# Kernel tuning notes

Hardware: AMD Instinct MI355X
Metric: run time of the kernel (lower is better)

Reference implementation:

```python
import jax, jax.numpy as jnp
import numpy as np


def setup_inputs() -> dict:
    key = jax.random.key(0)
    ks = jax.random.split(key, 8)
    B, C, H, W = 4, 256, 64, 64
    D = C // 8  # query/key dim = 32
    x = jax.random.normal(ks[0], (B, C, H, W), dtype=jnp.float32)
    # 1x1 convs == per-pixel linear maps over channels
    wq = jax.random.normal(ks[1], (D, C), dtype=jnp.float32) * 0.05
    bq = jnp.zeros((D,), dtype=jnp.float32)
    wk = jax.random.normal(ks[2], (D, C), dtype=jnp.float32) * 0.05
    bk = jnp.zeros((D,), dtype=jnp.float32)
    wv = jax.random.normal(ks[3], (C, C), dtype=jnp.float32) * 0.05
    bv = jnp.zeros((C,), dtype=jnp.float32)
    # gamma is initialized to 0 in the original; use a nonzero scalar so the
    # attention path actually contributes to the output / gradients.
    gamma = jnp.array([0.5], dtype=jnp.float32)
    return {"x": x, "wq": wq, "bq": bq, "wk": wk, "bk": bk,
            "wv": wv, "bv": bv, "gamma": gamma}


def reference(x, wq, bq, wk, bk, wv, bv, gamma):
    B, C, H, W = x.shape
    N = H * W
    xf = x.reshape(B, C, N)
    q = jnp.einsum('dc,bcn->bdn', wq, xf) + bq[:, None]   # [B, D, N]
    k = jnp.einsum('dc,bcn->bdn', wk, xf) + bk[:, None]   # [B, D, N]
    v = jnp.einsum('oc,bcn->bon', wv, xf) + bv[:, None]   # [B, C, N]
    # energy[b, i, j] = <q_i, k_j>; softmax over keys j (unscaled, as in source)
    energy = jnp.einsum('bdi,bdj->bij', q, k)             # [B, N, N]
    attn = jax.nn.softmax(energy, axis=-1)
    # out[b, c, j] = sum_i attn[b, i, j] * v[b, c, i]  (transposed aggregation,
    # matching bmm(attention.permute(0,2,1), value.permute(0,2,1)))
    out = jnp.einsum('bij,bci->bcj', attn, v)             # [B, C, N]
    out = out.reshape(B, C, H, W)
    return gamma[0] * out + x
```

## Files before the change

### kernel.cpp

```cpp
#include <hip/hip_runtime.h>

#define NB 4
#define CCH 256
#define NN 4096
#define DD 32

typedef __attribute__((ext_vector_type(8))) short bf16x8;
typedef __attribute__((ext_vector_type(8))) _Float16 f16x8;
typedef __attribute__((ext_vector_type(4))) _Float16 f16x4;
typedef __attribute__((ext_vector_type(2))) __fp16 fp16x2;
typedef __attribute__((ext_vector_type(4))) float f32x4;

#define MFB(a,b,c) __builtin_amdgcn_mfma_f32_16x16x32_bf16(a,b,c,0,0,0)
#define MFH(a,b,c) __builtin_amdgcn_mfma_f32_16x16x32_f16(a,b,c,0,0,0)
#define L2E 1.44269504f

__device__ inline unsigned short f2bf(float f){
    union { float f; unsigned u; } v; v.f = f;
    unsigned r = v.u + 0x7fffu + ((v.u >> 16) & 1u);
    return (unsigned short)(r >> 16);
}
__device__ inline float bfval(unsigned short h){
    union { unsigned u; float f; } v; v.u = ((unsigned)h) << 16; return v.f;
}
__device__ inline float vexp2(float x){
    float r; asm("v_exp_f32 %0, %1" : "=v"(r) : "v"(x)); return r;
}
__device__ inline f16x4 pk4(float p0, float p1, float p2, float p3){
    union { fp16x2 h2[2]; f16x4 v; } u;
    u.h2[0] = __builtin_amdgcn_cvt_pkrtz(p0, p1);
    u.h2[1] = __builtin_amdgcn_cvt_pkrtz(p2, p3);
    return u.v;
}

__global__ __launch_bounds__(256) void proj_qk(
    const float* __restrict__ x,
    const float* __restrict__ wq, const float* __restrict__ bq,
    const float* __restrict__ wk, const float* __restrict__ bk,
    _Float16* __restrict__ q16,
    _Float16* __restrict__ k_hi, _Float16* __restrict__ k_lo)
{
    const int t = threadIdx.x;
    const int w = t >> 6;
    const int l = t & 63;
    const int lr = l & 15, lg = l >> 4;
    const int nb = blockIdx.x;
    const int b  = blockIdx.y;
    const int n0 = nb*64 + w*16;
    const int n  = n0 + lr;

    const float* xb = x + (size_t)b*CCH*NN;

    f32x4 acc[4] = {};

    for (int kc = 0; kc < 8; kc++) {
        const int cbase = kc*32 + lg*8;
        float xv[8];
        #pragma unroll
        for (int e = 0; e < 8; e++)
            xv[e] = xb[(size_t)(cbase + e)*NN + n];
        bf16x8 xh, xl;
        #pragma unroll
        for (int e = 0; e < 8; e++) {
            unsigned short h = f2bf(xv[e]);
            xh[e] = (short)h;
            xl[e] = (short)f2bf(xv[e] - bfval(h));
        }
        #pragma unroll
        for (int f = 0; f < 4; f++) {
            const float* wrow = (f < 2) ? (wq + (size_t)(f*16 + lr)*CCH)
                                        : (wk + (size_t)((f-2)*16 + lr)*CCH);
            float4 a4 = *(const float4*)(wrow + cbase);
            float4 b4 = *(const float4*)(wrow + cbase + 4);
            float wv8[8] = {a4.x,a4.y,a4.z,a4.w,b4.x,b4.y,b4.z,b4.w};
            bf16x8 wh, wl;
            #pragma unroll
            for (int e = 0; e < 8; e++) {
                unsigned short h = f2bf(wv8[e]);
                wh[e] = (short)h;
                wl[e] = (short)f2bf(wv8[e] - bfval(h));
            }
            acc[f] = MFB(xh, wl, acc[f]);
            acc[f] = MFB(xl, wh, acc[f]);
            acc[f] = MFB(xh, wh, acc[f]);
        }
    }

    #pragma unroll
    for (int f = 0; f < 4; f++) {
        const int d = (f & 1)*16 + lr;
        const bool isq = (f < 2);
        float bias = isq ? bq[d] : bk[d];
        #pragma unroll
        for (int r = 0; r < 4; r++) {
            int nn = n0 + lg*4 + r;
            float val = acc[f][r] + bias;
            size_t a = ((size_t)(b*NN + nn))*DD + d;
            if (isq) {
                q16[a] = (_Float16)val;
            } else {
                _Float16 h = (_Float16)val;
                k_hi[a] = h;
                k_lo[a] = (_Float16)(val - (float)h);
            }
        }
    }
}

__global__ __launch_bounds__(512) void proj_v(
    const float* __restrict__ x,
    const float* __restrict__ wv, const float* __restrict__ bv,
    _Float16* __restrict__ v16)
{
    const int t = threadIdx.x;
    const int w = t >> 6;
    const int cg = w >> 2;
    const int ng = w & 3;
    const int l = t & 63;
    const int lr = l & 15, lg = l >> 4;
    const int ob = blockIdx.x;
    const int nb = blockIdx.y;
    const int b  = blockIdx.z;
    const int n0 = nb*64 + ng*16;
    const int n  = n0 + lr;
    const int cbase0 = ob*128 + cg*64;

    const float* xb = x + (size_t)b*CCH*NN;

    f32x4 acc[4] = {};

    for (int kc = 0; kc < 8; kc++) {
        const int kbase = kc*32 + lg*8;
        float xv[8];
        #pragma unroll
        for (int e = 0; e < 8; e++)
            xv[e] = xb[(size_t)(kbase + e)*NN + n];
        bf16x8 xh, xl;
        #pragma unroll
        for (int e = 0; e < 8; e++) {
            unsigned short h = f2bf(xv[e]);
            xh[e] = (short)h;
            xl[e] = (short)f2bf(xv[e] - bfval(h));
        }
        #pragma unroll
        for (int f = 0; f < 4; f++) {
            const float* wrow = wv + (size_t)(cbase0 + f*16 + lr)*CCH;
            float4 a4 = *(const float4*)(wrow + kbase);
            float4 b4 = *(const float4*)(wrow + kbase + 4);
            float wv8[8] = {a4.x,a4.y,a4.z,a4.w,b4.x,b4.y,b4.z,b4.w};
            bf16x8 wh, wl;
            #pragma unroll
            for (int e = 0; e < 8; e++) {
                unsigned short h = f2bf(wv8[e]);
                wh[e] = (short)h;
                wl[e] = (short)f2bf(wv8[e] - bfval(h));
            }
            acc[f] = MFB(wl, xh, acc[f]);
            acc[f] = MFB(wh, xl, acc[f]);
            acc[f] = MFB(wh, xh, acc[f]);
        }
    }

    const size_t bslice = (size_t)b*(NN/8);
    #pragma unroll
    for (int f = 0; f < 4; f++) {
        #pragma unroll
        for (int r = 0; r < 4; r++) {
            int c = cbase0 + f*16 + lg*4 + r;
            float val = acc[f][r] + bv[c];
            v16[(((bslice + (n >> 3))*CCH + c) << 3) + (n & 7)] = (_Float16)val;
        }
    }
}

__global__ __launch_bounds__(512) void stats_kernel(
    const _Float16* __restrict__ q16,
    const _Float16* __restrict__ kh, const _Float16* __restrict__ kl,
    float* __restrict__ Zp)
{
    __shared__ float zW[8][64];
    const int t = threadIdx.x;
    const int w = t >> 6;
    const int l = t & 63;
    const int lr = l & 15, lg = l >> 4;
    const int it = blockIdx.x;
    const int jc = blockIdx.y;
    const int b  = blockIdx.z;
    const int ibase = it*64;
    const f32x4 zero = {0.f,0.f,0.f,0.f};

    f16x8 qf[4];
    #pragma unroll
    for (int f = 0; f < 4; f++) {
        size_t a = ((size_t)(b*NN + ibase + f*16 + lr))*DD + lg*8;
        qf[f] = *(const f16x8*)(q16 + a);
    }
    float Z[4] = {0.f, 0.f, 0.f, 0.f};

    const size_t k0 = ((size_t)(b*NN + jc*2048 + w*16 + lr))*DD + lg*8;
    const _Float16* kp  = kh + k0;
    const _Float16* klp = kl + k0;

    for (int jt = 0; jt < 16; ++jt) {
        f16x8 kh2 = *(const f16x8*)kp;
        f16x8 kl2 = *(const f16x8*)klp;
        #pragma unroll
        for (int f = 0; f < 4; f++) {
            f32x4 e = MFH(kl2, qf[f], zero);
            e = MFH(kh2, qf[f], e);
            Z[f] += vexp2(e[0]*L2E) + vexp2(e[1]*L2E)
                  + vexp2(e[2]*L2E) + vexp2(e[3]*L2E);
        }
        kp  += 128*DD;
        klp += 128*DD;
    }
    #pragma unroll
    for (int f = 0; f < 4; f++) {
        Z[f] += __shfl_xor(Z[f], 16, 64);
        Z[f] += __shfl_xor(Z[f], 32, 64);
        if (lg == 0) zW[w][f*16 + lr] = Z[f];
    }
    __syncthreads();
    if (t < 64) {
        float z = 0.f;
        #pragma unroll
        for (int w2 = 0; w2 < 8; ++w2) z += zW[w2][t];
        Zp[((size_t)jc*NB + b)*NN + ibase + t] = z;
    }
}

__global__ __launch_bounds__(256) void combine_kernel(
    const float* __restrict__ Zp, float* __restrict__ Sx)
{
    const int idx = blockIdx.x*256 + threadIdx.x;
    Sx[idx] = log2f(Zp[idx] + Zp[(size_t)NB*NN + idx]);
}

__global__ __launch_bounds__(256, 2) void attn_kernel(
    const _Float16* __restrict__ q16,
    const _Float16* __restrict__ kh16, const _Float16* __restrict__ kl16,
    const _Float16* __restrict__ v16,
    const float* __restrict__ Sx,
    const float* __restrict__ x, const float* __restrict__ gamma,
    float* __restrict__ out)
{
    __shared__ __align__(16) f32x4 Rb[4096];

    const int t = threadIdx.x;
    const int wv = t >> 6;
    const int l = t & 63;
    const int lr = l & 15, lg = l >> 4;

    const int lin = blockIdx.x;
    const int slice = lin & 7;
    const int b   = slice >> 1;
    const int ct  = slice & 1;
    const int jt  = lin >> 3;
    const int jbase = jt*64, cbase = ct*128;

    f16x8 kfh[4], kfl[4];
    #pragma unroll
    for (int jf = 0; jf < 4; jf++) {
        size_t a = ((size_t)(b*NN + jbase + jf*16 + lr))*DD + lg*8;
        kfh[jf] = *(const f16x8*)(kh16 + a);
        kfl[jf] = *(const f16x8*)(kl16 + a);
    }

    const float* Sb = Sx + (size_t)b*NN;
    const _Float16* vb = v16 + (size_t)b*(NN/8)*CCH*8;

    const int i0 = wv*1024;

    const int sigma = 8*(lr >> 2) + (lr & 3);
    const _Float16* qpA = q16 + ((size_t)(b*NN + i0 + sigma))*DD + lg*8;
    const _Float16* qpB = qpA + 4*DD;
    const float* spA = Sb + i0 + 8*lg;
    const float* spB = spA + 4;
    const _Float16* vp = vb + (((size_t)(i0/8 + lg)*CCH + cbase + lr) << 3);

    f32x4 acc[4][8] = {};

    #pragma clang loop unroll(disable)
    for (int s = 0; s < 32; ++s) {
        f16x8 qA = *(const f16x8*)qpA;  qpA += 32*DD;
        f16x8 qB = *(const f16x8*)qpB;  qpB += 32*DD;
        float4 sA4 = *(const float4*)spA; spA += 32;
        float4 sB4 = *(const float4*)spB; spB += 32;
        f16x8 vv[8];
        #pragma unroll
        for (int cf = 0; cf < 8; cf++)
            vv[cf] = *(const f16x8*)(vp + cf*128);
        vp += 32*CCH;

        #pragma unroll
        for (int jf = 0; jf < 4; jf++) {
            f32x4 eA = {};
            eA = MFH(qA, kfl[jf], eA);
            eA = MFH(qA, kfh[jf], eA);
            f32x4 eB = {};
            eB = MFH(qB, kfl[jf], eB);
            eB = MFH(qB, kfh[jf], eB);
            union { f16x4 h4[2]; f16x8 h8; } pu;
            pu.h4[0] = pk4(vexp2(fmaf(eA[0], L2E, -sA4.x)),
                           vexp2(fmaf(eA[1], L2E, -sA4.y)),
                           vexp2(fmaf(eA[2], L2E, -sA4.z)),
                           vexp2(fmaf(eA[3], L2E, -sA4.w)));
            pu.h4[1] = pk4(vexp2(fmaf(eB[0], L2E, -sB4.x)),
                           vexp2(fmaf(eB[1], L2E, -sB4.y)),
                           vexp2(fmaf(eB[2], L2E, -sB4.z)),
                           vexp2(fmaf(eB[3], L2E, -sB4.w)));
            f16x8 pa = pu.h8;
            __builtin_amdgcn_s_setprio(1);
            #pragma unroll
            for (int cf = 0; cf < 8; cf++)
                acc[jf][cf] = MFH(pa, vv[cf], acc[jf][cf]);
            __builtin_amdgcn_s_setprio(0);
        }
    }

    if (wv == 2) {
        #pragma unroll
        for (int jf = 0; jf < 4; jf++)
            #pragma unroll
            for (int cf = 0; cf < 8; cf++)
                Rb[((jf*8 + cf) << 6) + l] = acc[jf][cf];
    } else if (wv == 3) {
        #pragma unroll
        for (int jf = 0; jf < 4; jf++)
            #pragma unroll
            for (int cf = 0; cf < 8; cf++)
                Rb[2048 + ((jf*8 + cf) << 6) + l] = acc[jf][cf];
    }
    __syncthreads();
    if (wv == 0) {
        #pragma unroll
        for (int jf = 0; jf < 4; jf++)
            #pragma unroll
            for (int cf = 0; cf < 8; cf++)
                acc[jf][cf] += Rb[((jf*8 + cf) << 6) + l];
    } else if (wv == 1) {
        #pragma unroll
        for (int jf = 0; jf < 4; jf++)
            #pragma unroll
            for (int cf = 0; cf < 8; cf++)
                acc[jf][cf] += Rb[2048 + ((jf*8 + cf) << 6) + l];
    }
    __syncthreads();
    if (wv == 0) {
        #pragma unroll
        for (int cf = 0; cf < 8; cf++) {
            Rb[((0*8 + cf) << 6) + l] = acc[2][cf];
            Rb[((1*8 + cf) << 6) + l] = acc[3][cf];
        }
    } else if (wv == 1) {
        #pragma unroll
        for (int cf = 0; cf < 8; cf++) {
            Rb[2048 + ((0*8 + cf) << 6) + l] = acc[0][cf];
            Rb[2048 + ((1*8 + cf) << 6) + l] = acc[1][cf];
        }
    }
    __syncthreads();

    const float gam = gamma[0];
    if (wv == 0) {
        #pragma unroll
        for (int cf = 0; cf < 8; cf++) {
            {
                f32x4 o = Rb[2048 + ((0*8 + cf) << 6) + l];
                f32x4 a = acc[0][cf];
                a[0]+=o[0]; a[1]+=o[1]; a[2]+=o[2]; a[3]+=o[3];
                const int c = cbase + cf*16 + lr;
                const int j = jbase + 0*16 + lg*4;
                size_t off = ((size_t)(b*CCH + c))*NN + j;
                float4 xv = *(const float4*)(x + off);
                float4 ov;
                ov.x = fmaf(gam, a[0], xv.x);
                ov.y = fmaf(gam, a[1], xv.y);
                ov.z = fmaf(gam, a[2], xv.z);
                ov.w = fmaf(gam, a[3], xv.w);
                *(float4*)(out + off) = ov;
            }
            {
                f32x4 o = Rb[2048 + ((1*8 + cf) << 6) + l];
                f32x4 a = acc[1][cf];
                a[0]+=o[0]; a[1]+=o[1]; a[2]+=o[2]; a[3]+=o[3];
                const int c = cbase + cf*16 + lr;
                const int j = jbase + 1*16 + lg*4;
                size_t off = ((size_t)(b*CCH + c))*NN + j;
                float4 xv = *(const float4*)(x + off);
                float4 ov;
                ov.x = fmaf(gam, a[0], xv.x);
                ov.y = fmaf(gam, a[1], xv.y);
                ov.z = fmaf(gam, a[2], xv.z);
                ov.w = fmaf(gam, a[3], xv.w);
                *(float4*)(out + off) = ov;
            }
        }
    } else if (wv == 1) {
        #pragma unroll
        for (int cf = 0; cf < 8; cf++) {
            {
                f32x4 o = Rb[((0*8 + cf) << 6) + l];
                f32x4 a = acc[2][cf];
                a[0]+=o[0]; a[1]+=o[1]; a[2]+=o[2]; a[3]+=o[3];
                const int c = cbase + cf*16 + lr;
                const int j = jbase + 2*16 + lg*4;
                size_t off = ((size_t)(b*CCH + c))*NN + j;
                float4 xv = *(const float4*)(x + off);
                float4 ov;
                ov.x = fmaf(gam, a[0], xv.x);
                ov.y = fmaf(gam, a[1], xv.y);
                ov.z = fmaf(gam, a[2], xv.z);
                ov.w = fmaf(gam, a[3], xv.w);
                *(float4*)(out + off) = ov;
            }
            {
                f32x4 o = Rb[((1*8 + cf) << 6) + l];
                f32x4 a = acc[3][cf];
                a[0]+=o[0]; a[1]+=o[1]; a[2]+=o[2]; a[3]+=o[3];
                const int c = cbase + cf*16 + lr;
                const int j = jbase + 3*16 + lg*4;
                size_t off = ((size_t)(b*CCH + c))*NN + j;
                float4 xv = *(const float4*)(x + off);
                float4 ov;
                ov.x = fmaf(gam, a[0], xv.x);
                ov.y = fmaf(gam, a[1], xv.y);
                ov.z = fmaf(gam, a[2], xv.z);
                ov.w = fmaf(gam, a[3], xv.w);
                *(float4*)(out + off) = ov;
            }
        }
    }
}

extern "C" void kernel_launch(void* const* d_in, const int* in_sizes, int n_in,
                              void* d_out, int out_size, void* d_ws, size_t ws_size,
                              hipStream_t stream)
{
    (void)in_sizes; (void)n_in; (void)out_size; (void)ws_size;
    const float* x     = (const float*)d_in[0];
    const float* wq    = (const float*)d_in[1];
    const float* bq    = (const float*)d_in[2];
    const float* wk    = (const float*)d_in[3];
    const float* bk    = (const float*)d_in[4];
    const float* wv    = (const float*)d_in[5];
    const float* bv    = (const float*)d_in[6];
    const float* gamma = (const float*)d_in[7];
    float* out = (float*)d_out;

    char* ws = (char*)d_ws;
    _Float16* q16  = (_Float16*)(ws + 0x000000);
    _Float16* k_hi = (_Float16*)(ws + 0x100000);
    _Float16* k_lo = (_Float16*)(ws + 0x200000);
    _Float16* v16  = (_Float16*)(ws + 0x400000);
    float*    Zp   = (float*)   (ws + 0xC00000);
    float*    Sx   = (float*)   (ws + 0xC20000);

    proj_qk<<<dim3(64, 4),    256, 0, stream>>>(x, wq, bq, wk, bk,
                                                q16, k_hi, k_lo);
    proj_v <<<dim3(2, 64, 4), 512, 0, stream>>>(x, wv, bv, v16);
    stats_kernel  <<<dim3(64, 2, 4), 512, 0, stream>>>(q16, k_hi, k_lo, Zp);
    combine_kernel<<<dim3(64),       256, 0, stream>>>(Zp, Sx);
    attn_kernel   <<<dim3(512),      256, 0, stream>>>(
        q16, k_hi, k_lo, v16, Sx, x, gamma, out);
}
```

Measured before the change: 118.6 us.

## Pre-split weights to bf16 hi/lo tiles, fuse softmax stats, batch attention MFMAs

Adds a small kernel that converts wq/wk/wv once into MFMA-tiled bf16 hi/lo arrays, so the projection kernels load ready fragments instead of redoing the fp32 split in every block. The stats kernel now covers all keys per block with 32 queries, which removes the partial-sum buffer and the separate combine launch at the cost of a longer serial loop per block. The attention inner loop computes all four P fragments before issuing the 32 PV MFMAs under one priority window, which raises register pressure in exchange for fewer priority toggles and better MFMA back-to-back issue.

```diff
diff --git a/kernel.cpp b/kernel.cpp
--- a/kernel.cpp
+++ b/kernel.cpp
@@ -33,10 +33,33 @@
     return u.v;
 }
 
+__global__ __launch_bounds__(256) void prep_w_blk(
+    const float* __restrict__ wq, const float* __restrict__ wk,
+    const float* __restrict__ wv,
+    unsigned short* __restrict__ wqh, unsigned short* __restrict__ wql,
+    unsigned short* __restrict__ wkh, unsigned short* __restrict__ wkl,
+    unsigned short* __restrict__ wvh, unsigned short* __restrict__ wvl)
+{
+    const int idx = blockIdx.x*256 + threadIdx.x;
+    const float* src; unsigned short *dh, *dl; int d, c;
+    if (idx < 8192)       { src = wq; dh = wqh; dl = wql; d = idx >> 8;           c = idx & 255; }
+    else if (idx < 16384) { src = wk; dh = wkh; dl = wkl; d = (idx-8192) >> 8;    c = idx & 255; }
+    else                  { src = wv; dh = wvh; dl = wvl; d = (idx-16384) >> 8;   c = idx & 255; }
+    float v = src[d*CCH + c];
+    const int tile = d >> 4, lr = d & 15;
+    const int kc = c >> 5, lg = (c >> 3) & 3, e = c & 7;
+    const int off = ((((tile*8 + kc)*4 + lg)*16) + lr)*8 + e;
+    unsigned short h = f2bf(v);
+    dh[off] = h;
+    dl[off] = f2bf(v - bfval(h));
+}
+
 __global__ __launch_bounds__(256) void proj_qk(
     const float* __restrict__ x,
-    const float* __restrict__ wq, const float* __restrict__ bq,
-    const float* __restrict__ wk, const float* __restrict__ bk,
+    const unsigned short* __restrict__ wqh, const unsigned short* __restrict__ wql,
+    const float* __restrict__ bq,
+    const unsigned short* __restrict__ wkh, const unsigned short* __restrict__ wkl,
+    const float* __restrict__ bk,
     _Float16* __restrict__ q16,
     _Float16* __restrict__ k_hi, _Float16* __restrict__ k_lo)
 {
@@ -68,18 +91,11 @@
         }
         #pragma unroll
         for (int f = 0; f < 4; f++) {
-            const float* wrow = (f < 2) ? (wq + (size_t)(f*16 + lr)*CCH)
-                                        : (wk + (size_t)((f-2)*16 + lr)*CCH);
-            float4 a4 = *(const float4*)(wrow + cbase);
-            float4 b4 = *(const float4*)(wrow + cbase + 4);
-            float wv8[8] = {a4.x,a4.y,a4.z,a4.w,b4.x,b4.y,b4.z,b4.w};
-            bf16x8 wh, wl;
-            #pragma unroll
-            for (int e = 0; e < 8; e++) {
-                unsigned short h = f2bf(wv8[e]);
-                wh[e] = (short)h;
-                wl[e] = (short)f2bf(wv8[e] - bfval(h));
-            }
+            const int off = ((((f & 1)*8 + kc)*4 + lg)*16 + lr)*8;
+            const unsigned short* ph = (f < 2) ? wqh : wkh;
+            const unsigned short* pl = (f < 2) ? wql : wkl;
+            bf16x8 wh = *(const bf16x8*)(ph + off);
+            bf16x8 wl = *(const bf16x8*)(pl + off);
             acc[f] = MFB(xh, wl, acc[f]);
             acc[f] = MFB(xl, wh, acc[f]);
             acc[f] = MFB(xh, wh, acc[f]);
@@ -109,7 +125,8 @@
 
 __global__ __launch_bounds__(512) void proj_v(
     const float* __restrict__ x,
-    const float* __restrict__ wv, const float* __restrict__ bv,
+    const unsigned short* __restrict__ wvh, const unsigned short* __restrict__ wvl,
+    const float* __restrict__ bv,
     _Float16* __restrict__ v16)
 {
     const int t = threadIdx.x;
@@ -124,6 +141,7 @@
     const int n0 = nb*64 + ng*16;
     const int n  = n0 + lr;
     const int cbase0 = ob*128 + cg*64;
+    const int ctile0 = ob*8 + cg*4;
 
     const float* xb = x + (size_t)b*CCH*NN;
 
@@ -144,17 +162,9 @@
         }
         #pragma unroll
         for (int f = 0; f < 4; f++) {
-            const float* wrow = wv + (size_t)(cbase0 + f*16 + lr)*CCH;
-            float4 a4 = *(const float4*)(wrow + kbase);
-            float4 b4 = *(const float4*)(wrow + kbase + 4);
-            float wv8[8] = {a4.x,a4.y,a4.z,a4.w,b4.x,b4.y,b4.z,b4.w};
-            bf16x8 wh, wl;
-            #pragma unroll
-            for (int e = 0; e < 8; e++) {
-                unsigned short h = f2bf(wv8[e]);
-                wh[e] = (short)h;
-                wl[e] = (short)f2bf(wv8[e] - bfval(h));
-            }
+            const int off = ((((ctile0 + f)*8 + kc)*4 + lg)*16 + lr)*8;
+            bf16x8 wh = *(const bf16x8*)(wvh + off);
+            bf16x8 wl = *(const bf16x8*)(wvl + off);
             acc[f] = MFB(wl, xh, acc[f]);
             acc[f] = MFB(wh, xl, acc[f]);
             acc[f] = MFB(wh, xh, acc[f]);
@@ -176,36 +186,35 @@
 __global__ __launch_bounds__(512) void stats_kernel(
     const _Float16* __restrict__ q16,
     const _Float16* __restrict__ kh, const _Float16* __restrict__ kl,
-    float* __restrict__ Zp)
-{
-    __shared__ float zW[8][64];
+    float* __restrict__ Sx)
+{
+    __shared__ float zW[8][32];
     const int t = threadIdx.x;
     const int w = t >> 6;
     const int l = t & 63;
     const int lr = l & 15, lg = l >> 4;
     const int it = blockIdx.x;
-    const int jc = blockIdx.y;
-    const int b  = blockIdx.z;
-    const int ibase = it*64;
+    const int b  = blockIdx.y;
+    const int ibase = it*32;
     const f32x4 zero = {0.f,0.f,0.f,0.f};
 
-    f16x8 qf[4];
+    f16x8 qf[2];
     #pragma unroll
-    for (int f = 0; f < 4; f++) {
+    for (int f = 0; f < 2; f++) {
         size_t a = ((size_t)(b*NN + ibase + f*16 + lr))*DD + lg*8;
         qf[f] = *(const f16x8*)(q16 + a);
     }
-    float Z[4] = {0.f, 0.f, 0.f, 0.f};
-
-    const size_t k0 = ((size_t)(b*NN + jc*2048 + w*16 + lr))*DD + lg*8;
+    float Z[2] = {0.f, 0.f};
+
+    const size_t k0 = ((size_t)(b*NN + w*16 + lr))*DD + lg*8;
     const _Float16* kp  = kh + k0;
     const _Float16* klp = kl + k0;
 
-    for (int jt = 0; jt < 16; ++jt) {
+    for (int jt = 0; jt < 32; ++jt) {
         f16x8 kh2 = *(const f16x8*)kp;
         f16x8 kl2 = *(const f16x8*)klp;
         #pragma unroll
-        for (int f = 0; f < 4; f++) {
+        for (int f = 0; f < 2; f++) {
             f32x4 e = MFH(kl2, qf[f], zero);
             e = MFH(kh2, qf[f], e);
             Z[f] += vexp2(e[0]*L2E) + vexp2(e[1]*L2E)
@@ -215,25 +224,18 @@
         klp += 128*DD;
     }
     #pragma unroll
-    for (int f = 0; f < 4; f++) {
+    for (int f = 0; f < 2; f++) {
         Z[f] += __shfl_xor(Z[f], 16, 64);
         Z[f] += __shfl_xor(Z[f], 32, 64);
         if (lg == 0) zW[w][f*16 + lr] = Z[f];
     }
     __syncthreads();
-    if (t < 64) {
+    if (t < 32) {
         float z = 0.f;
         #pragma unroll
         for (int w2 = 0; w2 < 8; ++w2) z += zW[w2][t];
-        Zp[((size_t)jc*NB + b)*NN + ibase + t] = z;
-    }
-}
-
-__global__ __launch_bounds__(256) void combine_kernel(
-    const float* __restrict__ Zp, float* __restrict__ Sx)
-{
-    const int idx = blockIdx.x*256 + threadIdx.x;
-    Sx[idx] = log2f(Zp[idx] + Zp[(size_t)NB*NN + idx]);
+        Sx[(size_t)b*NN + ibase + t] = log2f(z);
+    }
 }
 
 __global__ __launch_bounds__(256, 2) void attn_kernel(
@@ -292,6 +294,7 @@
             vv[cf] = *(const f16x8*)(vp + cf*128);
         vp += 32*CCH;
 
+        f16x8 pa[4];
         #pragma unroll
         for (int jf = 0; jf < 4; jf++) {
             f32x4 eA = {};
@@ -309,13 +312,16 @@
                            vexp2(fmaf(eB[1], L2E, -sB4.y)),
                            vexp2(fmaf(eB[2], L2E, -sB4.z)),
                            vexp2(fmaf(eB[3], L2E, -sB4.w)));
-            f16x8 pa = pu.h8;
-            __builtin_amdgcn_s_setprio(1);
+            pa[jf] = pu.h8;
+        }
+
+        __builtin_amdgcn_s_setprio(1);
+        #pragma unroll
+        for (int jf = 0; jf < 4; jf++)
             #pragma unroll
             for (int cf = 0; cf < 8; cf++)
-                acc[jf][cf] = MFH(pa, vv[cf], acc[jf][cf]);
-            __builtin_amdgcn_s_setprio(0);
-        }
+                acc[jf][cf] = MFH(pa[jf], vv[cf], acc[jf][cf]);
+        __builtin_amdgcn_s_setprio(0);
     }
 
     if (wv == 2) {
@@ -453,14 +459,20 @@
     _Float16* k_hi = (_Float16*)(ws + 0x100000);
     _Float16* k_lo = (_Float16*)(ws + 0x200000);
     _Float16* v16  = (_Float16*)(ws + 0x400000);
-    float*    Zp   = (float*)   (ws + 0xC00000);
-    float*    Sx   = (float*)   (ws + 0xC20000);
-
-    proj_qk<<<dim3(64, 4),    256, 0, stream>>>(x, wq, bq, wk, bk,
-                                                q16, k_hi, k_lo);
-    proj_v <<<dim3(2, 64, 4), 512, 0, stream>>>(x, wv, bv, v16);
-    stats_kernel  <<<dim3(64, 2, 4), 512, 0, stream>>>(q16, k_hi, k_lo, Zp);
-    combine_kernel<<<dim3(64),       256, 0, stream>>>(Zp, Sx);
-    attn_kernel   <<<dim3(512),      256, 0, stream>>>(
+    float*    Sx   = (float*)   (ws + 0xC00000);
+    unsigned short* wqh = (unsigned short*)(ws + 0xC10000);
+    unsigned short* wql = (unsigned short*)(ws + 0xC14000);
+    unsigned short* wkh = (unsigned short*)(ws + 0xC18000);
+    unsigned short* wkl = (unsigned short*)(ws + 0xC1C000);
+    unsigned short* wvh = (unsigned short*)(ws + 0xC20000);
+    unsigned short* wvl = (unsigned short*)(ws + 0xC40000);
+
+    prep_w_blk  <<<dim3(320),      256, 0, stream>>>(
+        wq, wk, wv, wqh, wql, wkh, wkl, wvh, wvl);
+    proj_qk     <<<dim3(64, 4),    256, 0, stream>>>(
+        x, wqh, wql, bq, wkh, wkl, bk, q16, k_hi, k_lo);
+    proj_v      <<<dim3(2, 64, 4), 512, 0, stream>>>(x, wvh, wvl, bv, v16);
+    stats_kernel<<<dim3(128, 4),   512, 0, stream>>>(q16, k_hi, k_lo, Sx);
+    attn_kernel <<<dim3(512),      256, 0, stream>>>(
         q16, k_hi, k_lo, v16, Sx, x, gamma, out);
 }
```

New measurement: 101.6 us. 14.3% less time.
